# Kernel tuning notes

Hardware: AMD Instinct MI355X
Metric: run time of the kernel (lower is better)

## Reference

```python
import jax, jax.numpy as jnp
import numpy as np

B, T, C = 4, 1024, 1024
H, L = 16, 256
D = C // H  # head_dim = 64


def setup_inputs() -> dict:
    key = jax.random.key(0)
    ks = jax.random.split(key, 10)
    s = lambda fan_in: 1.0 / np.sqrt(fan_in)
    return {
        "x": jax.random.normal(ks[0], (B, T, C), jnp.float32),
        "padding_mask": jax.random.randint(ks[1], (B, T), 0, 2, jnp.int32),
        "interaction_matrix": jax.random.normal(ks[2], (B, T, T, H), jnp.float32),
        # weights stored [in, out] (x @ W == torch Linear with W = weight.T)
        "W_ckv": jax.random.uniform(ks[3], (C, L), jnp.float32, -s(C), s(C)),
        "W_cq": jax.random.uniform(ks[4], (C, L), jnp.float32, -s(C), s(C)),
        "W_kc": jax.random.uniform(ks[5], (L, C), jnp.float32, -s(L), s(L)),
        "W_qc": jax.random.uniform(ks[6], (L, C), jnp.float32, -s(L), s(L)),
        "W_vc": jax.random.uniform(ks[7], (L, C), jnp.float32, -s(L), s(L)),
        "W_proj": jax.random.uniform(ks[8], (C, C), jnp.float32, -s(C), s(C)),
        "b_proj": jax.random.uniform(ks[9], (C,), jnp.float32, -s(C), s(C)),
    }


def reference(x, padding_mask, interaction_matrix, W_ckv, W_cq, W_kc, W_qc, W_vc, W_proj, b_proj):
    # low-rank down/up projections
    kv_down = x @ W_ckv                      # [B,T,L]
    q_down = x @ W_cq                        # [B,T,L]
    k = (kv_down @ W_kc).reshape(B, T, H, D).transpose(0, 2, 1, 3)  # [B,H,T,D]
    q = (q_down @ W_qc).reshape(B, T, H, D).transpose(0, 2, 1, 3)
    v = (kv_down @ W_vc).reshape(B, T, H, D).transpose(0, 2, 1, 3)

    scores = jnp.einsum("bhqd,bhkd->bhqk", q, k) * (D ** -0.5)      # [B,H,T,T]

    # padding mask (fix=False path): mask[b,t]==0 masks query row t, fill -1e9
    row_mask = padding_mask[:, None, :, None]                        # [B,1,T,1]
    scores = jnp.where(row_mask == 0, jnp.float32(-1e9), scores)

    # causal mask
    causal = jnp.tril(jnp.ones((T, T), jnp.bool_))
    scores = jnp.where(causal, scores, -jnp.inf)

    # additive interaction bias: [B,T,T,H].transpose(1,3) -> [B,H,T,T]
    scores = scores + interaction_matrix.transpose(0, 3, 2, 1)

    attn = jax.nn.softmax(scores, axis=-1)                           # dropout=0 (eval)
    ctx = jnp.einsum("bhqk,bhkd->bhqd", attn, v)                     # [B,H,T,D]
    ctx = ctx.transpose(0, 2, 1, 3).reshape(B, T, C)
    return ctx @ W_proj + b_proj
```

## Files before the change

### kernel.cpp

```cpp
#include <hip/hip_runtime.h>

typedef unsigned short u16;
typedef unsigned int u32;
typedef __attribute__((ext_vector_type(8))) __bf16 bf16x8;
typedef __attribute__((ext_vector_type(4))) float f32x4;
typedef __attribute__((ext_vector_type(4))) short s16x4;

#define LOG2E 1.4426950408889634f
#define NINF (-__builtin_inff())

static constexpr size_t OFF_WT_CKV = 0;
static constexpr size_t OFF_WT_CQ  = 262144;
static constexpr size_t OFF_WT_KC  = 524288;
static constexpr size_t OFF_WT_QC  = 786432;
static constexpr size_t OFF_WT_VC  = 1048576;
static constexpr size_t OFF_WT_PROJ= 1310720;
static constexpr size_t OFF_XBF    = 2359296;
static constexpr size_t OFF_DQ     = OFF_XBF + 4194304;
static constexpr size_t OFF_KB     = OFF_DQ  + 2097152;
static constexpr size_t OFF_QB     = OFF_KB  + 4194304;
static constexpr size_t OFF_VTB    = OFF_QB  + 4194304;
static constexpr size_t OFF_CTX    = OFF_XBF;

__device__ __forceinline__ u16 f2bf(float f) {
  u32 u = __builtin_bit_cast(u32, f);
  u = (u + 0x7fffu + ((u >> 16) & 1u)) >> 16;
  return (u16)u;
}

__device__ __forceinline__ void gld16(const void* g, void* l) {
  __builtin_amdgcn_global_load_lds(
      (const __attribute__((address_space(1))) u32*)(unsigned long long)g,
      (__attribute__((address_space(3))) u32*)(u32)(unsigned long long)l,
      16, 0, 0);
}

__global__ __launch_bounds__(256) void convert_kernel(
    const float* __restrict__ xin, const float* __restrict__ w0,
    const float* __restrict__ w1, const float* __restrict__ w2,
    const float* __restrict__ w3, const float* __restrict__ w4,
    const float* __restrict__ w5, u16* __restrict__ ws) {
  int id = blockIdx.x * 256 + threadIdx.x;
  if (id < 4194304) { ws[OFF_XBF + id] = f2bf(xin[id]); return; }
  id -= 4194304;
  if (id < 262144) { int k = id >> 8, n = id & 255;
    ws[OFF_WT_CKV + (size_t)n*1024 + k] = f2bf(w0[id]); return; }
  id -= 262144;
  if (id < 262144) { int k = id >> 8, n = id & 255;
    ws[OFF_WT_CQ + (size_t)n*1024 + k] = f2bf(w1[id]); return; }
  id -= 262144;
  if (id < 262144) { int k = id >> 10, n = id & 1023;
    ws[OFF_WT_KC + (size_t)n*256 + k] = f2bf(w2[id]); return; }
  id -= 262144;
  if (id < 262144) { int k = id >> 10, n = id & 1023;
    ws[OFF_WT_QC + (size_t)n*256 + k] = f2bf(w3[id]); return; }
  id -= 262144;
  if (id < 262144) { int k = id >> 10, n = id & 1023;
    ws[OFF_WT_VC + (size_t)n*256 + k] = f2bf(w4[id]); return; }
  id -= 262144;
  if (id < 1048576) { int k = id >> 10, n = id & 1023;
    ws[OFF_WT_PROJ + (size_t)n*1024 + k] = f2bf(w5[id]); return; }
}

template<int MODE>
__global__ __launch_bounds__(256, 2) void gemm_kernel(
    const u16* __restrict__ A, const u16* __restrict__ BT,
    u16* __restrict__ ws, float* __restrict__ out, const float* __restrict__ bias) {
  constexpr int KDIM = (MODE == 1) ? 256 : 1024;
  constexpr int LDA  = (MODE == 1) ? 512 : 1024;
  __shared__ u16 lA[128*32];
  __shared__ u16 lB[128*32];
  const int t = threadIdx.x;
  const int lane = t & 63;
  const int c = lane & 15, quad = lane >> 4;
  const int w = t >> 6, wr = w >> 1, wc = w & 1;
  const int gm0 = blockIdx.y * 128, ct0 = blockIdx.x * 128;
  const u16* Ae = A;
  int out_id = 0;
  if (MODE == 1) { out_id = ct0 >> 10; if (out_id == 1) Ae += 256; }
  const int m0s = t >> 2, q0s = t & 3;
  const int m1s = m0s + 64;

  f32x4 acc[4][4];
  #pragma unroll
  for (int i = 0; i < 4; ++i)
    #pragma unroll
    for (int j = 0; j < 4; ++j) acc[i][j] = (f32x4)0.0f;

  for (int k0 = 0; k0 < KDIM; k0 += 32) {
    __syncthreads();
    gld16(Ae + (size_t)(gm0 + m0s)*LDA + k0 + q0s*8, (char*)lA + t*16);
    gld16(Ae + (size_t)(gm0 + m1s)*LDA + k0 + q0s*8, (char*)lA + (t+256)*16);
    gld16(BT + (size_t)(ct0 + m0s)*KDIM + k0 + q0s*8, (char*)lB + t*16);
    gld16(BT + (size_t)(ct0 + m1s)*KDIM + k0 + q0s*8, (char*)lB + (t+256)*16);
    __syncthreads();
    bf16x8 af[4], bfr[4];
    #pragma unroll
    for (int mt = 0; mt < 4; ++mt)
      af[mt] = *(const bf16x8*)(lA + (wr*64 + mt*16 + c)*32 + quad*8);
    #pragma unroll
    for (int nt = 0; nt < 4; ++nt)
      bfr[nt] = *(const bf16x8*)(lB + (wc*64 + nt*16 + c)*32 + quad*8);
    #pragma unroll
    for (int mt = 0; mt < 4; ++mt)
      #pragma unroll
      for (int nt = 0; nt < 4; ++nt)
        acc[mt][nt] = __builtin_amdgcn_mfma_f32_16x16x32_bf16(af[mt], bfr[nt], acc[mt][nt], 0, 0, 0);
  }

  const int rbase = gm0 + wr*64;
  const int cbase = ct0 + wc*64;
  if (MODE == 0) {
    #pragma unroll
    for (int mt = 0; mt < 4; ++mt)
      #pragma unroll
      for (int nt = 0; nt < 4; ++nt)
        #pragma unroll
        for (int j = 0; j < 4; ++j) {
          int row = rbase + mt*16 + quad*4 + j;
          int col = cbase + nt*16 + c;
          ws[OFF_DQ + (size_t)row*512 + col] = f2bf(acc[mt][nt][j]);
        }
  } else if (MODE == 2) {
    float bv[4];
    #pragma unroll
    for (int nt = 0; nt < 4; ++nt) bv[nt] = bias[cbase + nt*16 + c];
    #pragma unroll
    for (int mt = 0; mt < 4; ++mt)
      #pragma unroll
      for (int nt = 0; nt < 4; ++nt)
        #pragma unroll
        for (int j = 0; j < 4; ++j) {
          int row = rbase + mt*16 + quad*4 + j;
          out[(size_t)row*1024 + cbase + nt*16 + c] = acc[mt][nt][j] + bv[nt];
        }
  } else {
    const int cl = (ct0 & 1023) + wc*64;
    const int hcol = cl >> 6;
    if (out_id == 2) {
      #pragma unroll
      for (int mt = 0; mt < 4; ++mt) {
        int row0 = rbase + mt*16 + quad*4;
        int bb = row0 >> 10, t0 = row0 & 1023;
        #pragma unroll
        for (int nt = 0; nt < 4; ++nt) {
          int d = nt*16 + c;
          s16x4 pk;
          #pragma unroll
          for (int j = 0; j < 4; ++j) pk[j] = (short)f2bf(acc[mt][nt][j]);
          *(s16x4*)(ws + OFF_VTB + (((size_t)bb*16 + hcol)*64 + d)*1024 + t0) = pk;
        }
      }
    } else {
      const float sc = out_id ? 0.125f : 1.0f;
      const size_t base = out_id ? OFF_QB : OFF_KB;
      #pragma unroll
      for (int mt = 0; mt < 4; ++mt)
        #pragma unroll
        for (int nt = 0; nt < 4; ++nt)
          #pragma unroll
          for (int j = 0; j < 4; ++j) {
            int row = rbase + mt*16 + quad*4 + j;
            int bb = row >> 10, tt = row & 1023;
            ws[base + ((((size_t)bb*16 + hcol)*1024 + tt)<<6) + nt*16 + c]
                = f2bf(acc[mt][nt][j]*sc);
          }
    }
  }
}

__global__ __launch_bounds__(512, 4) void attn_kernel(
    const u16* __restrict__ Kb, const u16* __restrict__ Qb,
    const u16* __restrict__ VTb, u16* __restrict__ ctx,
    const float* __restrict__ im, const int* __restrict__ pmask) {
  __shared__ float lim[32*132];
  __shared__ u16   lp[8][16*40];
  typedef __attribute__((ext_vector_type(4))) float float4v;

  const int t = threadIdx.x, lane = t & 63, w = t >> 6;
  const int c = lane & 15, quad = lane >> 4;
  const int bi = blockIdx.x;
  const int xcd = bi & 7, b = xcd >> 1, p0 = xcd & 1;
  const int hh = (bi >> 3) & 1, hi = bi >> 4;
  const int qt = 63 - ((hi << 1) | p0);
  const int h0 = hh * 8, h = h0 + w;
  const int qmax = qt*16 + 15;
  const int ktmax = qmax >> 5;
  const size_t bh = ((size_t)b*16 + h) << 16;

  bf16x8 qf0 = *(const bf16x8*)(Qb + bh + (size_t)(qt*16 + c)*64 + quad*8);
  bf16x8 qf1 = *(const bf16x8*)(Qb + bh + (size_t)(qt*16 + c)*64 + 32 + quad*8);

  int tq[4], rm[4];
  #pragma unroll
  for (int j = 0; j < 4; ++j) {
    tq[j] = qt*16 + quad*4 + j;
    rm[j] = pmask[b*1024 + tq[j]];
  }
  float mr[4] = {NINF, NINF, NINF, NINF};
  float lr[4] = {0.f, 0.f, 0.f, 0.f};
  f32x4 O[4] = {(f32x4)0.f, (f32x4)0.f, (f32x4)0.f, (f32x4)0.f};

  for (int kt = 0; kt <= ktmax; ++kt) {
    const int kb = kt*32;
    const int nk = min(32, qmax + 1 - kb);
    __syncthreads();
    #pragma unroll
    for (int i = 0; i < 2; ++i) {
      int s = i*512 + t;
      int k = s >> 5, sub = s & 31, q = sub >> 1, hp = (sub & 1)*4;
      if (k < nk) {
        float4v v = __builtin_nontemporal_load((const float4v*)(
            im + (((size_t)b*1024 + kb + k)*1024 + qt*16 + q)*16 + h0 + hp));
        *(float4v*)(lim + k*132 + q*8 + hp) = v;
      }
    }
    __syncthreads();

    f32x4 S[2] = {(f32x4)0.f, (f32x4)0.f};
    #pragma unroll
    for (int nt = 0; nt < 2; ++nt) {
      const u16* kp = Kb + bh + (size_t)(kb + nt*16 + c)*64 + quad*8;
      bf16x8 kf0 = *(const bf16x8*)kp;
      bf16x8 kf1 = *(const bf16x8*)(kp + 32);
      S[nt] = __builtin_amdgcn_mfma_f32_16x16x32_bf16(qf0, kf0, S[nt], 0, 0, 0);
      S[nt] = __builtin_amdgcn_mfma_f32_16x16x32_bf16(qf1, kf1, S[nt], 0, 0, 0);
    }
    #pragma unroll
    for (int nt = 0; nt < 2; ++nt) {
      int tk = kb + nt*16 + c;
      #pragma unroll
      for (int j = 0; j < 4; ++j) {
        float s = S[nt][j] + lim[(nt*16 + c)*132 + (quad*4 + j)*8 + w];
        s = rm[j] ? s : 0.0f;
        s = (tk <= tq[j]) ? s : NINF;
        S[nt][j] = s;
      }
    }
    float mn[4], al[4];
    #pragma unroll
    for (int j = 0; j < 4; ++j) {
      float vm = fmaxf(S[0][j], S[1][j]);
      vm = fmaxf(vm, __shfl_xor(vm, 1, 64));
      vm = fmaxf(vm, __shfl_xor(vm, 2, 64));
      vm = fmaxf(vm, __shfl_xor(vm, 4, 64));
      vm = fmaxf(vm, __shfl_xor(vm, 8, 64));
      mn[j] = fmaxf(mr[j], vm);
      al[j] = exp2f((mr[j] - mn[j]) * LOG2E);
      mr[j] = mn[j];
    }
    float p[2][4];
    #pragma unroll
    for (int nt = 0; nt < 2; ++nt)
      #pragma unroll
      for (int j = 0; j < 4; ++j)
        p[nt][j] = exp2f((S[nt][j] - mn[j]) * LOG2E);
    #pragma unroll
    for (int j = 0; j < 4; ++j) {
      float sum = p[0][j] + p[1][j];
      sum += __shfl_xor(sum, 1, 64);
      sum += __shfl_xor(sum, 2, 64);
      sum += __shfl_xor(sum, 4, 64);
      sum += __shfl_xor(sum, 8, 64);
      lr[j] = lr[j]*al[j] + sum;
    }
    #pragma unroll
    for (int nd = 0; nd < 4; ++nd)
      #pragma unroll
      for (int j = 0; j < 4; ++j) O[nd][j] *= al[j];
    #pragma unroll
    for (int nt = 0; nt < 2; ++nt)
      #pragma unroll
      for (int j = 0; j < 4; ++j)
        lp[w][(quad*4 + j)*40 + nt*16 + c] = f2bf(p[nt][j]);
    bf16x8 pf = *(const bf16x8*)&lp[w][c*40 + quad*8];
    #pragma unroll
    for (int nd = 0; nd < 4; ++nd) {
      bf16x8 vf = *(const bf16x8*)(VTb + bh + (size_t)(nd*16 + c)*1024 + kb + quad*8);
      O[nd] = __builtin_amdgcn_mfma_f32_16x16x32_bf16(pf, vf, O[nd], 0, 0, 0);
    }
  }

  float inv[4];
  #pragma unroll
  for (int j = 0; j < 4; ++j) inv[j] = 1.0f / lr[j];
  #pragma unroll
  for (int nd = 0; nd < 4; ++nd)
    #pragma unroll
    for (int j = 0; j < 4; ++j)
      ctx[((size_t)b*1024 + tq[j])*1024 + h*64 + nd*16 + c] = f2bf(O[nd][j] * inv[j]);
}

extern "C" void kernel_launch(void* const* d_in, const int* in_sizes, int n_in,
                              void* d_out, int out_size, void* d_ws, size_t ws_size,
                              hipStream_t stream) {
  const float* x     = (const float*)d_in[0];
  const int*   pm    = (const int*)d_in[1];
  const float* im    = (const float*)d_in[2];
  const float* wckv  = (const float*)d_in[3];
  const float* wcq   = (const float*)d_in[4];
  const float* wkc   = (const float*)d_in[5];
  const float* wqc   = (const float*)d_in[6];
  const float* wvc   = (const float*)d_in[7];
  const float* wproj = (const float*)d_in[8];
  const float* bproj = (const float*)d_in[9];
  u16* ws = (u16*)d_ws;
  float* out = (float*)d_out;

  convert_kernel<<<25600, 256, 0, stream>>>(x, wckv, wcq, wkc, wqc, wvc, wproj, ws);
  gemm_kernel<0><<<dim3(4, 32), 256, 0, stream>>>(ws + OFF_XBF, ws + OFF_WT_CKV, ws, nullptr, nullptr);
  gemm_kernel<1><<<dim3(24, 32), 256, 0, stream>>>(ws + OFF_DQ, ws + OFF_WT_KC, ws, nullptr, nullptr);
  attn_kernel<<<512, 512, 0, stream>>>(ws + OFF_KB, ws + OFF_QB, ws + OFF_VTB,
                                       ws + OFF_CTX, im, pm);
  gemm_kernel<2><<<dim3(8, 32), 256, 0, stream>>>(ws + OFF_CTX, ws + OFF_WT_PROJ, ws, out, bproj);
}
```

Baseline: 526.2 us.

## Pair causal query tiles per block, prefetch bias, vectorize x convert, retile GEMMs

The attention kernel now runs two query tiles per block, one long and one short (63-p and p), to balance causal work. It halves the grid and register-prefetches the next interaction-matrix tile while the current one is being consumed. The x-to-bf16 conversion is vectorized to 8 elements per thread. The GEMMs are templated on tile size, so the down-projection uses 64x64 tiles and the output projection uses 64x128 tiles for more blocks. The risks are lower attention occupancy (launch bounds 2), fewer attention blocks, and the bias tile staying resident in registers.

Result: faster. 477.2 us (-9.3%).

```diff
diff --git a/kernel.cpp b/kernel.cpp
--- a/kernel.cpp
+++ b/kernel.cpp
@@ -5,6 +5,7 @@
 typedef __attribute__((ext_vector_type(8))) __bf16 bf16x8;
 typedef __attribute__((ext_vector_type(4))) float f32x4;
 typedef __attribute__((ext_vector_type(4))) short s16x4;
+typedef __attribute__((ext_vector_type(4))) u32 u32x4;
 
 #define LOG2E 1.4426950408889634f
 #define NINF (-__builtin_inff())
@@ -40,9 +41,20 @@
     const float* __restrict__ w1, const float* __restrict__ w2,
     const float* __restrict__ w3, const float* __restrict__ w4,
     const float* __restrict__ w5, u16* __restrict__ ws) {
-  int id = blockIdx.x * 256 + threadIdx.x;
-  if (id < 4194304) { ws[OFF_XBF + id] = f2bf(xin[id]); return; }
-  id -= 4194304;
+  int gid = blockIdx.x * 256 + threadIdx.x;
+  if (gid < 524288) {
+    int i0 = gid * 8;
+    f32x4 a = *(const f32x4*)(xin + i0);
+    f32x4 b = *(const f32x4*)(xin + i0 + 4);
+    u32x4 pv;
+    pv[0] = (u32)f2bf(a[0]) | ((u32)f2bf(a[1]) << 16);
+    pv[1] = (u32)f2bf(a[2]) | ((u32)f2bf(a[3]) << 16);
+    pv[2] = (u32)f2bf(b[0]) | ((u32)f2bf(b[1]) << 16);
+    pv[3] = (u32)f2bf(b[2]) | ((u32)f2bf(b[3]) << 16);
+    *(u32x4*)(ws + OFF_XBF + i0) = pv;
+    return;
+  }
+  int id = gid - 524288;
   if (id < 262144) { int k = id >> 8, n = id & 255;
     ws[OFF_WT_CKV + (size_t)n*1024 + k] = f2bf(w0[id]); return; }
   id -= 262144;
@@ -62,59 +74,62 @@
     ws[OFF_WT_PROJ + (size_t)n*1024 + k] = f2bf(w5[id]); return; }
 }
 
-template<int MODE>
-__global__ __launch_bounds__(256, 2) void gemm_kernel(
+template<int MODE, int MT, int NT>
+__global__ __launch_bounds__(256, (MT == 128) ? 2 : 4) void gemm_kernel(
     const u16* __restrict__ A, const u16* __restrict__ BT,
     u16* __restrict__ ws, float* __restrict__ out, const float* __restrict__ bias) {
   constexpr int KDIM = (MODE == 1) ? 256 : 1024;
   constexpr int LDA  = (MODE == 1) ? 512 : 1024;
-  __shared__ u16 lA[128*32];
-  __shared__ u16 lB[128*32];
+  constexpr int MW = MT / 32;
+  constexpr int NW = NT / 32;
+  __shared__ u16 lA[MT*32];
+  __shared__ u16 lB[NT*32];
   const int t = threadIdx.x;
   const int lane = t & 63;
   const int c = lane & 15, quad = lane >> 4;
   const int w = t >> 6, wr = w >> 1, wc = w & 1;
-  const int gm0 = blockIdx.y * 128, ct0 = blockIdx.x * 128;
+  const int gm0 = blockIdx.y * MT, ct0 = blockIdx.x * NT;
   const u16* Ae = A;
   int out_id = 0;
   if (MODE == 1) { out_id = ct0 >> 10; if (out_id == 1) Ae += 256; }
   const int m0s = t >> 2, q0s = t & 3;
-  const int m1s = m0s + 64;
-
-  f32x4 acc[4][4];
+
+  f32x4 acc[MW][NW];
   #pragma unroll
-  for (int i = 0; i < 4; ++i)
-    #pragma unroll
-    for (int j = 0; j < 4; ++j) acc[i][j] = (f32x4)0.0f;
+  for (int i = 0; i < MW; ++i)
+    #pragma unroll
+    for (int j = 0; j < NW; ++j) acc[i][j] = (f32x4)0.0f;
 
   for (int k0 = 0; k0 < KDIM; k0 += 32) {
     __syncthreads();
     gld16(Ae + (size_t)(gm0 + m0s)*LDA + k0 + q0s*8, (char*)lA + t*16);
-    gld16(Ae + (size_t)(gm0 + m1s)*LDA + k0 + q0s*8, (char*)lA + (t+256)*16);
+    if (MT == 128)
+      gld16(Ae + (size_t)(gm0 + m0s + 64)*LDA + k0 + q0s*8, (char*)lA + (t+256)*16);
     gld16(BT + (size_t)(ct0 + m0s)*KDIM + k0 + q0s*8, (char*)lB + t*16);
-    gld16(BT + (size_t)(ct0 + m1s)*KDIM + k0 + q0s*8, (char*)lB + (t+256)*16);
+    if (NT == 128)
+      gld16(BT + (size_t)(ct0 + m0s + 64)*KDIM + k0 + q0s*8, (char*)lB + (t+256)*16);
     __syncthreads();
-    bf16x8 af[4], bfr[4];
-    #pragma unroll
-    for (int mt = 0; mt < 4; ++mt)
-      af[mt] = *(const bf16x8*)(lA + (wr*64 + mt*16 + c)*32 + quad*8);
-    #pragma unroll
-    for (int nt = 0; nt < 4; ++nt)
-      bfr[nt] = *(const bf16x8*)(lB + (wc*64 + nt*16 + c)*32 + quad*8);
-    #pragma unroll
-    for (int mt = 0; mt < 4; ++mt)
-      #pragma unroll
-      for (int nt = 0; nt < 4; ++nt)
+    bf16x8 af[MW], bfr[NW];
+    #pragma unroll
+    for (int mt = 0; mt < MW; ++mt)
+      af[mt] = *(const bf16x8*)(lA + (wr*(MT/2) + mt*16 + c)*32 + quad*8);
+    #pragma unroll
+    for (int nt = 0; nt < NW; ++nt)
+      bfr[nt] = *(const bf16x8*)(lB + (wc*(NT/2) + nt*16 + c)*32 + quad*8);
+    #pragma unroll
+    for (int mt = 0; mt < MW; ++mt)
+      #pragma unroll
+      for (int nt = 0; nt < NW; ++nt)
         acc[mt][nt] = __builtin_amdgcn_mfma_f32_16x16x32_bf16(af[mt], bfr[nt], acc[mt][nt], 0, 0, 0);
   }
 
-  const int rbase = gm0 + wr*64;
-  const int cbase = ct0 + wc*64;
+  const int rbase = gm0 + wr*(MT/2);
+  const int cbase = ct0 + wc*(NT/2);
   if (MODE == 0) {
     #pragma unroll
-    for (int mt = 0; mt < 4; ++mt)
-      #pragma unroll
-      for (int nt = 0; nt < 4; ++nt)
+    for (int mt = 0; mt < MW; ++mt)
+      #pragma unroll
+      for (int nt = 0; nt < NW; ++nt)
         #pragma unroll
         for (int j = 0; j < 4; ++j) {
           int row = rbase + mt*16 + quad*4 + j;
@@ -122,13 +137,13 @@
           ws[OFF_DQ + (size_t)row*512 + col] = f2bf(acc[mt][nt][j]);
         }
   } else if (MODE == 2) {
-    float bv[4];
-    #pragma unroll
-    for (int nt = 0; nt < 4; ++nt) bv[nt] = bias[cbase + nt*16 + c];
-    #pragma unroll
-    for (int mt = 0; mt < 4; ++mt)
-      #pragma unroll
-      for (int nt = 0; nt < 4; ++nt)
+    float bv[NW];
+    #pragma unroll
+    for (int nt = 0; nt < NW; ++nt) bv[nt] = bias[cbase + nt*16 + c];
+    #pragma unroll
+    for (int mt = 0; mt < MW; ++mt)
+      #pragma unroll
+      for (int nt = 0; nt < NW; ++nt)
         #pragma unroll
         for (int j = 0; j < 4; ++j) {
           int row = rbase + mt*16 + quad*4 + j;
@@ -139,11 +154,11 @@
     const int hcol = cl >> 6;
     if (out_id == 2) {
       #pragma unroll
-      for (int mt = 0; mt < 4; ++mt) {
+      for (int mt = 0; mt < MW; ++mt) {
         int row0 = rbase + mt*16 + quad*4;
         int bb = row0 >> 10, t0 = row0 & 1023;
         #pragma unroll
-        for (int nt = 0; nt < 4; ++nt) {
+        for (int nt = 0; nt < NW; ++nt) {
           int d = nt*16 + c;
           s16x4 pk;
           #pragma unroll
@@ -155,9 +170,9 @@
       const float sc = out_id ? 0.125f : 1.0f;
       const size_t base = out_id ? OFF_QB : OFF_KB;
       #pragma unroll
-      for (int mt = 0; mt < 4; ++mt)
-        #pragma unroll
-        for (int nt = 0; nt < 4; ++nt)
+      for (int mt = 0; mt < MW; ++mt)
+        #pragma unroll
+        for (int nt = 0; nt < NW; ++nt)
           #pragma unroll
           for (int j = 0; j < 4; ++j) {
             int row = rbase + mt*16 + quad*4 + j;
@@ -169,126 +184,134 @@
   }
 }
 
-__global__ __launch_bounds__(512, 4) void attn_kernel(
+__global__ __launch_bounds__(512, 2) void attn_kernel(
     const u16* __restrict__ Kb, const u16* __restrict__ Qb,
     const u16* __restrict__ VTb, u16* __restrict__ ctx,
     const float* __restrict__ im, const int* __restrict__ pmask) {
-  __shared__ float lim[32*132];
+  __shared__ float lim[32*196];
   __shared__ u16   lp[8][16*40];
-  typedef __attribute__((ext_vector_type(4))) float float4v;
 
   const int t = threadIdx.x, lane = t & 63, w = t >> 6;
   const int c = lane & 15, quad = lane >> 4;
   const int bi = blockIdx.x;
-  const int xcd = bi & 7, b = xcd >> 1, p0 = xcd & 1;
-  const int hh = (bi >> 3) & 1, hi = bi >> 4;
-  const int qt = 63 - ((hi << 1) | p0);
-  const int h0 = hh * 8, h = h0 + w;
-  const int qmax = qt*16 + 15;
-  const int ktmax = qmax >> 5;
+  const int g = bi >> 4, hh = (bi >> 3) & 1, s = bi & 7;
+  const int b = s >> 1, pair = g*2 + (s & 1);
+  const int h0 = hh*8, h = h0 + w;
   const size_t bh = ((size_t)b*16 + h) << 16;
 
-  bf16x8 qf0 = *(const bf16x8*)(Qb + bh + (size_t)(qt*16 + c)*64 + quad*8);
-  bf16x8 qf1 = *(const bf16x8*)(Qb + bh + (size_t)(qt*16 + c)*64 + 32 + quad*8);
-
-  int tq[4], rm[4];
-  #pragma unroll
-  for (int j = 0; j < 4; ++j) {
-    tq[j] = qt*16 + quad*4 + j;
-    rm[j] = pmask[b*1024 + tq[j]];
+  const int k0s = t >> 5, q0s = (t & 31) >> 1, hp0 = (t & 1) * 4;
+  const float* imb = im + ((size_t)b << 24) + h0;
+  float* l0 = lim + k0s*196 + q0s*12 + hp0;
+  float* l1 = lim + (k0s + 16)*196 + q0s*12 + hp0;
+
+  const int qtA = 63 - pair;
+  f32x4 r0 = *(const f32x4*)(imb + (((size_t)k0s)*1024 + qtA*16 + q0s)*16 + hp0);
+  f32x4 r1 = *(const f32x4*)(imb + (((size_t)(k0s+16))*1024 + qtA*16 + q0s)*16 + hp0);
+
+  for (int pass = 0; pass < 2; ++pass) {
+    const int qt = pass ? pair : qtA;
+    const int qrow0 = qt * 16;
+    const int ktmax = (qrow0 + 15) >> 5;
+
+    bf16x8 qf0 = *(const bf16x8*)(Qb + bh + (size_t)(qrow0 + c)*64 + quad*8);
+    bf16x8 qf1 = *(const bf16x8*)(Qb + bh + (size_t)(qrow0 + c)*64 + 32 + quad*8);
+
+    int tq[4], rm[4];
+    #pragma unroll
+    for (int j = 0; j < 4; ++j) {
+      tq[j] = qrow0 + quad*4 + j;
+      rm[j] = pmask[b*1024 + tq[j]];
+    }
+    float mr[4] = {NINF, NINF, NINF, NINF};
+    float lr[4] = {0.f, 0.f, 0.f, 0.f};
+    f32x4 O[4] = {(f32x4)0.f, (f32x4)0.f, (f32x4)0.f, (f32x4)0.f};
+
+    for (int kt = 0; kt <= ktmax; ++kt) {
+      const int kb = kt*32;
+      __syncthreads();
+      *(f32x4*)l0 = r0;
+      *(f32x4*)l1 = r1;
+      __syncthreads();
+      if (kt < ktmax) {
+        r0 = *(const f32x4*)(imb + (((size_t)(kb + 32 + k0s))*1024 + qrow0 + q0s)*16 + hp0);
+        r1 = *(const f32x4*)(imb + (((size_t)(kb + 48 + k0s))*1024 + qrow0 + q0s)*16 + hp0);
+      } else if (pass == 0) {
+        r0 = *(const f32x4*)(imb + (((size_t)k0s)*1024 + pair*16 + q0s)*16 + hp0);
+        r1 = *(const f32x4*)(imb + (((size_t)(k0s+16))*1024 + pair*16 + q0s)*16 + hp0);
+      }
+
+      f32x4 S[2] = {(f32x4)0.f, (f32x4)0.f};
+      #pragma unroll
+      for (int nt = 0; nt < 2; ++nt) {
+        const u16* kp = Kb + bh + (size_t)(kb + nt*16 + c)*64 + quad*8;
+        bf16x8 kf0 = *(const bf16x8*)kp;
+        bf16x8 kf1 = *(const bf16x8*)(kp + 32);
+        S[nt] = __builtin_amdgcn_mfma_f32_16x16x32_bf16(qf0, kf0, S[nt], 0, 0, 0);
+        S[nt] = __builtin_amdgcn_mfma_f32_16x16x32_bf16(qf1, kf1, S[nt], 0, 0, 0);
+      }
+      #pragma unroll
+      for (int nt = 0; nt < 2; ++nt) {
+        int tk = kb + nt*16 + c;
+        #pragma unroll
+        for (int j = 0; j < 4; ++j) {
+          float sv = S[nt][j] + lim[(nt*16 + c)*196 + (quad*4 + j)*12 + w];
+          sv = rm[j] ? sv : 0.0f;
+          sv = (tk <= tq[j]) ? sv : NINF;
+          S[nt][j] = sv;
+        }
+      }
+      float mn[4], al[4];
+      #pragma unroll
+      for (int j = 0; j < 4; ++j) {
+        float vm = fmaxf(S[0][j], S[1][j]);
+        vm = fmaxf(vm, __shfl_xor(vm, 1, 64));
+        vm = fmaxf(vm, __shfl_xor(vm, 2, 64));
+        vm = fmaxf(vm, __shfl_xor(vm, 4, 64));
+        vm = fmaxf(vm, __shfl_xor(vm, 8, 64));
+        mn[j] = fmaxf(mr[j], vm);
+        al[j] = exp2f((mr[j] - mn[j]) * LOG2E);
+        mr[j] = mn[j];
+      }
+      #pragma unroll
+      for (int nt = 0; nt < 2; ++nt)
+        #pragma unroll
+        for (int j = 0; j < 4; ++j)
+          S[nt][j] = exp2f((S[nt][j] - mn[j]) * LOG2E);
+      #pragma unroll
+      for (int j = 0; j < 4; ++j) {
+        float sum = S[0][j] + S[1][j];
+        sum += __shfl_xor(sum, 1, 64);
+        sum += __shfl_xor(sum, 2, 64);
+        sum += __shfl_xor(sum, 4, 64);
+        sum += __shfl_xor(sum, 8, 64);
+        lr[j] = lr[j]*al[j] + sum;
+      }
+      #pragma unroll
+      for (int nd = 0; nd < 4; ++nd)
+        #pragma unroll
+        for (int j = 0; j < 4; ++j) O[nd][j] *= al[j];
+      #pragma unroll
+      for (int nt = 0; nt < 2; ++nt)
+        #pragma unroll
+        for (int j = 0; j < 4; ++j)
+          lp[w][(quad*4 + j)*40 + nt*16 + c] = f2bf(S[nt][j]);
+      bf16x8 pf = *(const bf16x8*)&lp[w][c*40 + quad*8];
+      #pragma unroll
+      for (int nd = 0; nd < 4; ++nd) {
+        bf16x8 vf = *(const bf16x8*)(VTb + bh + (size_t)(nd*16 + c)*1024 + kb + quad*8);
+        O[nd] = __builtin_amdgcn_mfma_f32_16x16x32_bf16(pf, vf, O[nd], 0, 0, 0);
+      }
+    }
+
+    float inv[4];
+    #pragma unroll
+    for (int j = 0; j < 4; ++j) inv[j] = 1.0f / lr[j];
+    #pragma unroll
+    for (int nd = 0; nd < 4; ++nd)
+      #pragma unroll
+      for (int j = 0; j < 4; ++j)
+        ctx[((size_t)b*1024 + tq[j])*1024 + h*64 + nd*16 + c] = f2bf(O[nd][j] * inv[j]);
   }
-  float mr[4] = {NINF, NINF, NINF, NINF};
-  float lr[4] = {0.f, 0.f, 0.f, 0.f};
-  f32x4 O[4] = {(f32x4)0.f, (f32x4)0.f, (f32x4)0.f, (f32x4)0.f};
-
-  for (int kt = 0; kt <= ktmax; ++kt) {
-    const int kb = kt*32;
-    const int nk = min(32, qmax + 1 - kb);
-    __syncthreads();
-    #pragma unroll
-    for (int i = 0; i < 2; ++i) {
-      int s = i*512 + t;
-      int k = s >> 5, sub = s & 31, q = sub >> 1, hp = (sub & 1)*4;
-      if (k < nk) {
-        float4v v = __builtin_nontemporal_load((const float4v*)(
-            im + (((size_t)b*1024 + kb + k)*1024 + qt*16 + q)*16 + h0 + hp));
-        *(float4v*)(lim + k*132 + q*8 + hp) = v;
-      }
-    }
-    __syncthreads();
-
-    f32x4 S[2] = {(f32x4)0.f, (f32x4)0.f};
-    #pragma unroll
-    for (int nt = 0; nt < 2; ++nt) {
-      const u16* kp = Kb + bh + (size_t)(kb + nt*16 + c)*64 + quad*8;
-      bf16x8 kf0 = *(const bf16x8*)kp;
-      bf16x8 kf1 = *(const bf16x8*)(kp + 32);
-      S[nt] = __builtin_amdgcn_mfma_f32_16x16x32_bf16(qf0, kf0, S[nt], 0, 0, 0);
-      S[nt] = __builtin_amdgcn_mfma_f32_16x16x32_bf16(qf1, kf1, S[nt], 0, 0, 0);
-    }
-    #pragma unroll
-    for (int nt = 0; nt < 2; ++nt) {
-      int tk = kb + nt*16 + c;
-      #pragma unroll
-      for (int j = 0; j < 4; ++j) {
-        float s = S[nt][j] + lim[(nt*16 + c)*132 + (quad*4 + j)*8 + w];
-        s = rm[j] ? s : 0.0f;
-        s = (tk <= tq[j]) ? s : NINF;
-        S[nt][j] = s;
-      }
-    }
-    float mn[4], al[4];
-    #pragma unroll
-    for (int j = 0; j < 4; ++j) {
-      float vm = fmaxf(S[0][j], S[1][j]);
-      vm = fmaxf(vm, __shfl_xor(vm, 1, 64));
-      vm = fmaxf(vm, __shfl_xor(vm, 2, 64));
-      vm = fmaxf(vm, __shfl_xor(vm, 4, 64));
-      vm = fmaxf(vm, __shfl_xor(vm, 8, 64));
-      mn[j] = fmaxf(mr[j], vm);
-      al[j] = exp2f((mr[j] - mn[j]) * LOG2E);
-      mr[j] = mn[j];
-    }
-    float p[2][4];
-    #pragma unroll
-    for (int nt = 0; nt < 2; ++nt)
-      #pragma unroll
-      for (int j = 0; j < 4; ++j)
-        p[nt][j] = exp2f((S[nt][j] - mn[j]) * LOG2E);
-    #pragma unroll
-    for (int j = 0; j < 4; ++j) {
-      float sum = p[0][j] + p[1][j];
-      sum += __shfl_xor(sum, 1, 64);
-      sum += __shfl_xor(sum, 2, 64);
-      sum += __shfl_xor(sum, 4, 64);
-      sum += __shfl_xor(sum, 8, 64);
-      lr[j] = lr[j]*al[j] + sum;
-    }
-    #pragma unroll
-    for (int nd = 0; nd < 4; ++nd)
-      #pragma unroll
-      for (int j = 0; j < 4; ++j) O[nd][j] *= al[j];
-    #pragma unroll
-    for (int nt = 0; nt < 2; ++nt)
-      #pragma unroll
-      for (int j = 0; j < 4; ++j)
-        lp[w][(quad*4 + j)*40 + nt*16 + c] = f2bf(p[nt][j]);
-    bf16x8 pf = *(const bf16x8*)&lp[w][c*40 + quad*8];
-    #pragma unroll
-    for (int nd = 0; nd < 4; ++nd) {
-      bf16x8 vf = *(const bf16x8*)(VTb + bh + (size_t)(nd*16 + c)*1024 + kb + quad*8);
-      O[nd] = __builtin_amdgcn_mfma_f32_16x16x32_bf16(pf, vf, O[nd], 0, 0, 0);
-    }
-  }
-
-  float inv[4];
-  #pragma unroll
-  for (int j = 0; j < 4; ++j) inv[j] = 1.0f / lr[j];
-  #pragma unroll
-  for (int nd = 0; nd < 4; ++nd)
-    #pragma unroll
-    for (int j = 0; j < 4; ++j)
-      ctx[((size_t)b*1024 + tq[j])*1024 + h*64 + nd*16 + c] = f2bf(O[nd][j] * inv[j]);
 }
 
 extern "C" void kernel_launch(void* const* d_in, const int* in_sizes, int n_in,
@@ -307,10 +330,10 @@
   u16* ws = (u16*)d_ws;
   float* out = (float*)d_out;
 
-  convert_kernel<<<25600, 256, 0, stream>>>(x, wckv, wcq, wkc, wqc, wvc, wproj, ws);
-  gemm_kernel<0><<<dim3(4, 32), 256, 0, stream>>>(ws + OFF_XBF, ws + OFF_WT_CKV, ws, nullptr, nullptr);
-  gemm_kernel<1><<<dim3(24, 32), 256, 0, stream>>>(ws + OFF_DQ, ws + OFF_WT_KC, ws, nullptr, nullptr);
-  attn_kernel<<<512, 512, 0, stream>>>(ws + OFF_KB, ws + OFF_QB, ws + OFF_VTB,
+  convert_kernel<<<11264, 256, 0, stream>>>(x, wckv, wcq, wkc, wqc, wvc, wproj, ws);
+  gemm_kernel<0,64,64><<<dim3(8, 64), 256, 0, stream>>>(ws + OFF_XBF, ws + OFF_WT_CKV, ws, nullptr, nullptr);
+  gemm_kernel<1,128,128><<<dim3(24, 32), 256, 0, stream>>>(ws + OFF_DQ, ws + OFF_WT_KC, ws, nullptr, nullptr);
+  attn_kernel<<<256, 512, 0, stream>>>(ws + OFF_KB, ws + OFF_QB, ws + OFF_VTB,
                                        ws + OFF_CTX, im, pm);
-  gemm_kernel<2><<<dim3(8, 32), 256, 0, stream>>>(ws + OFF_CTX, ws + OFF_WT_PROJ, ws, out, bproj);
-}
+  gemm_kernel<2,64,128><<<dim3(8, 64), 256, 0, stream>>>(ws + OFF_CTX, ws + OFF_WT_PROJ, ws, out, bproj);
+}
```
